# Kernel tuning notes

Measured on AMD Instinct MI355X. Metric: run time of the kernel, lower is better.

The kernel has to match this reference:

```python
import jax, jax.numpy as jnp
import numpy as np


def setup_inputs() -> dict:
    key = jax.random.key(0)
    T, B, I, H = 512, 64, 512, 512
    k = 1.0 / np.sqrt(H)
    ks = jax.random.split(key, 5)
    x = jax.random.normal(ks[0], (T, B, I), dtype=jnp.float32)
    w_ih = jax.random.uniform(ks[1], (H, I), jnp.float32, -k, k)
    w_hh = jax.random.uniform(ks[2], (H, H), jnp.float32, -k, k)
    b_ih = jax.random.uniform(ks[3], (H,), jnp.float32, -k, k)
    b_hh = jax.random.uniform(ks[4], (H,), jnp.float32, -k, k)
    return {"x": x, "w_ih": w_ih, "w_hh": w_hh, "b_ih": b_ih, "b_hh": b_hh}


def reference(x, w_ih, w_hh, b_ih, b_hh):
    # Single-layer Elman RNN, batch_first=False: x is [T, B, I].
    # h_t = tanh(x_t @ W_ih^T + b_ih + h_{t-1} @ W_hh^T + b_hh)
    T, B, _ = x.shape
    H = w_hh.shape[0]
    # Precompute input projections for all timesteps in one big GEMM.
    xproj = jnp.einsum('tbi,hi->tbh', x, w_ih) + b_ih + b_hh  # [T, B, H]

    def step(h, xp_t):
        h_new = jnp.tanh(xp_t + h @ w_hh.T)
        return h_new, h_new

    h0 = jnp.zeros((B, H), dtype=x.dtype)
    h_n, output = jax.lax.scan(step, h0, xproj)
    # torch-style h_n has a leading num_layers dim
    return output, h_n[None]
```

## Files before the change

kernel.cpp:

```cpp
#include <hip/hip_runtime.h>
#include <hip/hip_fp16.h>

#define T_STEPS 512
#define BATCH   64
#define HID     512

#define SCH_REG  40
#define SCH_LDS  10
#define SCH_SA   7
#define SCH_SB   7

#define X16_OFF   0u
#define X16_BYTES (16777216u * 2u)
#define WIH_OFF   (X16_OFF + X16_BYTES)
#define WIH_BYTES (262144u * 2u)
#define WHH_OFF   (WIH_OFF + WIH_BYTES)
#define WHH_BYTES (262144u * 2u)
#define WS_FULL   (WHH_OFF + WHH_BYTES)

typedef _Float16 half2v  __attribute__((ext_vector_type(2)));
typedef short    short8  __attribute__((ext_vector_type(8)));
typedef float    f32x4   __attribute__((ext_vector_type(4)));
union F4H { float4 f; half2v h[4]; };

__device__ inline float dot2f(half2v a, half2v b, float c) {
    return __builtin_amdgcn_fdot2(a, b, c, false);
}
__device__ inline unsigned short f2bf(float f) {
    unsigned u = __builtin_bit_cast(unsigned, f);
    return (unsigned short)((u + 0x7FFFu + ((u >> 16) & 1u)) >> 16);
}

__global__ __launch_bounds__(256) void cvt_f16(const float* __restrict__ w,
                                               __half* __restrict__ o) {
    const int i = (blockIdx.x * 256 + threadIdx.x) * 4;
    float4 v = *(const float4*)(w + i);
    __half2 p0; p0.x = __float2half(v.x); p0.y = __float2half(v.y);
    __half2 p1; p1.x = __float2half(v.z); p1.y = __float2half(v.w);
    *(__half2*)(o + i)     = p0;
    *(__half2*)(o + i + 2) = p1;
}

__global__ __launch_bounds__(256) void cvt_bf16(const float* __restrict__ s,
                                                unsigned short* __restrict__ o) {
    const int i = (blockIdx.x * 256 + threadIdx.x) * 4;
    float4 v = *(const float4*)(s + i);
    ushort4 r = {f2bf(v.x), f2bf(v.y), f2bf(v.z), f2bf(v.w)};
    *(ushort4*)(o + i) = r;
}

__global__ __launch_bounds__(256) void xproj_mfma(
    const unsigned short* __restrict__ x16,
    const unsigned short* __restrict__ w16,
    const float* __restrict__ b_ih, const float* __restrict__ b_hh,
    float* __restrict__ out)
{
    __shared__ __align__(16) unsigned short As[128][40];
    __shared__ __align__(16) unsigned short Bs[128][40];

    const int tid   = threadIdx.x;
    const int mBase = blockIdx.y * 128;
    const int nBase = blockIdx.x * 128;
    const int wave  = tid >> 6, lane = tid & 63;
    const int wy    = wave >> 1, wx = wave & 1;
    const int quad  = lane >> 4, l15 = lane & 15;
    const int lr    = tid >> 2;
    const int lk    = (tid & 3) * 8;

    f32x4 acc[4][4] = {};

    const size_t arow0 = (size_t)(mBase + lr) * 512 + lk;
    const size_t brow0 = (size_t)(nBase + lr) * 512 + lk;

    for (int k0 = 0; k0 < 512; k0 += 32) {
        int4 a0 = *(const int4*)(x16 + arow0 + k0);
        int4 a1 = *(const int4*)(x16 + arow0 + (size_t)64 * 512 + k0);
        int4 b0 = *(const int4*)(w16 + brow0 + k0);
        int4 b1 = *(const int4*)(w16 + brow0 + (size_t)64 * 512 + k0);
        __syncthreads();
        *(int4*)&As[lr][lk]      = a0;
        *(int4*)&As[lr + 64][lk] = a1;
        *(int4*)&Bs[lr][lk]      = b0;
        *(int4*)&Bs[lr + 64][lk] = b1;
        __syncthreads();

        short8 af[4], bf[4];
#pragma unroll
        for (int mt = 0; mt < 4; ++mt)
            af[mt] = *(const short8*)&As[wy * 64 + mt * 16 + l15][quad * 8];
#pragma unroll
        for (int nt = 0; nt < 4; ++nt)
            bf[nt] = *(const short8*)&Bs[wx * 64 + nt * 16 + l15][quad * 8];
#pragma unroll
        for (int mt = 0; mt < 4; ++mt)
#pragma unroll
            for (int nt = 0; nt < 4; ++nt)
                acc[mt][nt] = __builtin_amdgcn_mfma_f32_16x16x32_bf16(
                    af[mt], bf[nt], acc[mt][nt], 0, 0, 0);
    }

    float bias[4]; int coln[4];
#pragma unroll
    for (int nt = 0; nt < 4; ++nt) {
        coln[nt] = nBase + wx * 64 + nt * 16 + l15;
        bias[nt] = b_ih[coln[nt]] + b_hh[coln[nt]];
    }
#pragma unroll
    for (int mt = 0; mt < 4; ++mt)
#pragma unroll
        for (int r = 0; r < 4; ++r) {
            const int row = mBase + wy * 64 + mt * 16 + quad * 4 + r;
#pragma unroll
            for (int nt = 0; nt < 4; ++nt)
                out[(size_t)row * 512 + coln[nt]] = acc[mt][nt][r] + bias[nt];
        }
}

__global__ __launch_bounds__(256) void xproj_gemm(
    const float* __restrict__ x, const float* __restrict__ w_ih,
    const float* __restrict__ b_ih, const float* __restrict__ b_hh,
    float* __restrict__ out)
{
    __shared__ __align__(16) float As[16][68];
    __shared__ __align__(16) float Bs[16][68];

    const int tid   = threadIdx.x;
    const int tx    = tid & 15;
    const int ty    = tid >> 4;
    const int mBase = blockIdx.y * 64;
    const int nBase = blockIdx.x * 64;
    const int ldr   = tid >> 2;
    const int ldk   = (tid & 3) * 4;

    float acc[4][4] = {};
    const float* aptr = x    + (size_t)(mBase + ldr) * 512 + ldk;
    const float* bptr = w_ih + (size_t)(nBase + ldr) * 512 + ldk;

    for (int k0 = 0; k0 < 512; k0 += 16) {
        float4 av = *(const float4*)(aptr + k0);
        float4 bv = *(const float4*)(bptr + k0);
        __syncthreads();
        As[ldk + 0][ldr] = av.x; As[ldk + 1][ldr] = av.y;
        As[ldk + 2][ldr] = av.z; As[ldk + 3][ldr] = av.w;
        Bs[ldk + 0][ldr] = bv.x; Bs[ldk + 1][ldr] = bv.y;
        Bs[ldk + 2][ldr] = bv.z; Bs[ldk + 3][ldr] = bv.w;
        __syncthreads();
#pragma unroll
        for (int kk = 0; kk < 16; ++kk) {
            float4 a = *(const float4*)&As[kk][ty * 4];
            float4 b = *(const float4*)&Bs[kk][tx * 4];
            float ar[4] = {a.x, a.y, a.z, a.w};
            float br[4] = {b.x, b.y, b.z, b.w};
#pragma unroll
            for (int i = 0; i < 4; ++i)
#pragma unroll
                for (int j = 0; j < 4; ++j)
                    acc[i][j] = fmaf(ar[i], br[j], acc[i][j]);
        }
    }
    const int n0 = nBase + tx * 4;
    float bias[4];
#pragma unroll
    for (int j = 0; j < 4; ++j) bias[j] = b_ih[n0 + j] + b_hh[n0 + j];
#pragma unroll
    for (int i = 0; i < 4; ++i) {
        const int m = mBase + ty * 4 + i;
        float4 v = {acc[i][0] + bias[0], acc[i][1] + bias[1],
                    acc[i][2] + bias[2], acc[i][3] + bias[3]};
        *(float4*)(out + (size_t)m * 512 + n0) = v;
    }
}

#define ACC4(WF, G) do {                                        \
    F4H hh_; hh_.f = *(const float4*)(hrow + (G) * 8);          \
    F4H ww_; ww_.f = (WF);                                      \
    a0 = dot2f(ww_.h[0], hh_.h[0], a0);                         \
    a1 = dot2f(ww_.h[1], hh_.h[1], a1);                         \
    a2 = dot2f(ww_.h[2], hh_.h[2], a2);                         \
    a3 = dot2f(ww_.h[3], hh_.h[3], a3); } while (0)

__global__ __launch_bounds__(512)
__attribute__((amdgpu_waves_per_eu(2, 2)))
void rnn_scan4(const __half* __restrict__ w16, float* __restrict__ out)
{
    __shared__ __align__(16) float4 wlds[SCH_LDS][HID];
    __shared__ __align__(16) __half hbuf[2][HID];

    const int b = blockIdx.x;
    const int j = threadIdx.x;

    const __half* wrow = w16 + (size_t)j * HID;

    float4 wreg[SCH_REG];
#pragma unroll
    for (int c = 0; c < SCH_REG; ++c)
        wreg[c] = *(const float4*)(wrow + c * 8);

#pragma unroll
    for (int c = 0; c < SCH_LDS; ++c)
        wlds[c][j] = *(const float4*)(wrow + (SCH_REG + c) * 8);

    hbuf[0][j] = __float2half(0.f);
    __syncthreads();

    float* outb = out + (size_t)b * HID + j;
    const size_t stride = (size_t)BATCH * HID;
    const __half* wstr = wrow + (SCH_REG + SCH_LDS) * 8;

    int cur = 0;
    float hn = 0.f;
    float xp_next = outb[0];

    for (int t = 0; t < T_STEPS; ++t) {
        const float xp = xp_next;
        const int tn = (t + 1 < T_STEPS) ? (t + 1) : t;
        xp_next = outb[(size_t)tn * stride];

        const __half* hrow = hbuf[cur];

        float4 wa[SCH_SA];
#pragma unroll
        for (int c = 0; c < SCH_SA; ++c)
            wa[c] = *(const float4*)(wstr + c * 8);

        float a0 = xp, a1 = 0.f, a2 = 0.f, a3 = 0.f;

#pragma unroll
        for (int c = 0; c < 20; ++c) ACC4(wreg[c], c);

#pragma unroll
        for (int c = 0; c < SCH_SA; ++c)
            ACC4(wa[c], SCH_REG + SCH_LDS + c);

        float4 wb[SCH_SB];
#pragma unroll
        for (int c = 0; c < SCH_SB; ++c)
            wb[c] = *(const float4*)(wstr + (SCH_SA + c) * 8);

#pragma unroll
        for (int c = 20; c < SCH_REG; ++c) ACC4(wreg[c], c);
#pragma unroll
        for (int c = 0; c < SCH_LDS; ++c) {
            float4 wf = wlds[c][j];
            ACC4(wf, SCH_REG + c);
        }

#pragma unroll
        for (int c = 0; c < SCH_SB; ++c)
            ACC4(wb[c], SCH_REG + SCH_LDS + SCH_SA + c);

        float s = (a0 + a1) + (a2 + a3);
        s = fminf(fmaxf(s, -15.f), 15.f);
        const float e = __expf(2.f * s);
        hn = (e - 1.f) * __builtin_amdgcn_rcpf(e + 1.f);

        outb[(size_t)t * stride] = hn;
        hbuf[cur ^ 1][j] = __float2half(hn);
        __syncthreads();
        cur ^= 1;
    }
    out[(size_t)T_STEPS * stride + (size_t)b * HID + j] = hn;
}

__global__ __launch_bounds__(512) void rnn_scan_f32(const float* __restrict__ w,
                                                    float* __restrict__ out)
{
    __shared__ __align__(16) __half hs[2][HID];
    const int b = blockIdx.x;
    const int j = threadIdx.x;

    hs[0][j] = __float2half(0.f);
    __syncthreads();

    const float* wrow32 = w + (size_t)j * HID;
    float* outb = out + (size_t)b * HID + j;
    int cur = 0;
    float hn = 0.f;

    for (int t = 0; t < T_STEPS; ++t) {
        float a0 = outb[(size_t)t * (BATCH * HID)];
        float a1 = 0.f, a2 = 0.f, a3 = 0.f;
#pragma unroll 4
        for (int k0 = 0; k0 < HID; k0 += 8) {
            float4 w0 = *(const float4*)(wrow32 + k0);
            float4 w1 = *(const float4*)(wrow32 + k0 + 4);
            F4H h; h.f = *(const float4*)(&hs[cur][k0]);
            float2 h0 = __half22float2(*(__half2*)&h.h[0]);
            float2 h1 = __half22float2(*(__half2*)&h.h[1]);
            float2 h2 = __half22float2(*(__half2*)&h.h[2]);
            float2 h3 = __half22float2(*(__half2*)&h.h[3]);
            a0 = fmaf(w0.x, h0.x, a0); a1 = fmaf(w0.y, h0.y, a1);
            a2 = fmaf(w0.z, h1.x, a2); a3 = fmaf(w0.w, h1.y, a3);
            a0 = fmaf(w1.x, h2.x, a0); a1 = fmaf(w1.y, h2.y, a1);
            a2 = fmaf(w1.z, h3.x, a2); a3 = fmaf(w1.w, h3.y, a3);
        }
        hn = tanhf((a0 + a1) + (a2 + a3));
        outb[(size_t)t * (BATCH * HID)] = hn;
        hs[cur ^ 1][j] = __float2half(hn);
        __syncthreads();
        cur ^= 1;
    }
    out[(size_t)T_STEPS * BATCH * HID + (size_t)b * HID + j] = hn;
}

extern "C" void kernel_launch(void* const* d_in, const int* in_sizes, int n_in,
                              void* d_out, int out_size, void* d_ws, size_t ws_size,
                              hipStream_t stream) {
    const float* x    = (const float*)d_in[0];
    const float* w_ih = (const float*)d_in[1];
    const float* w_hh = (const float*)d_in[2];
    const float* b_ih = (const float*)d_in[3];
    const float* b_hh = (const float*)d_in[4];
    float* out = (float*)d_out;

    char* ws = (char*)d_ws;
    const bool full = ws_size >= (size_t)WS_FULL;
    const bool mid  = ws_size >= (size_t)WHH_BYTES;

    if (full) {
        unsigned short* x16   = (unsigned short*)(ws + X16_OFF);
        unsigned short* wih16 = (unsigned short*)(ws + WIH_OFF);
        __half*         whh16 = (__half*)(ws + WHH_OFF);
        cvt_bf16<<<16384, 256, 0, stream>>>(x, x16);
        cvt_bf16<<<256,   256, 0, stream>>>(w_ih, wih16);
        cvt_f16 <<<256,   256, 0, stream>>>(w_hh, whh16);
        xproj_mfma<<<dim3(4, 256), 256, 0, stream>>>(x16, wih16, b_ih, b_hh, out);
        rnn_scan4<<<BATCH, HID, 0, stream>>>(whh16, out);
    } else if (mid) {
        __half* whh16 = (__half*)ws;
        cvt_f16<<<256, 256, 0, stream>>>(w_hh, whh16);
        xproj_gemm<<<dim3(8, 512), 256, 0, stream>>>(x, w_ih, b_ih, b_hh, out);
        rnn_scan4<<<BATCH, HID, 0, stream>>>(whh16, out);
    } else {
        xproj_gemm<<<dim3(8, 512), 256, 0, stream>>>(x, w_ih, b_ih, b_hh, out);
        rnn_scan_f32<<<BATCH, HID, 0, stream>>>(w_hh, out);
    }
}
```

Before: 892.5 us.

## Fuse x bf16 conversion into GEMM and transpose W_hh for coalesced streaming

The separate pass that converts x to bf16 is removed, and the GEMM now loads fp32 x and converts it while staging into LDS. This drops a 32MB write and a 32MB read of the temporary. W_hh is converted into a chunk-major transposed fp16 layout so that per-step weight streaming in the scan is coalesced across threads. The register/LDS split in the scan is rebalanced (36 register chunks, 14 LDS chunks), with asm barriers to keep the weights pinned in VGPRs. The workspace path and the middle fallback are simplified.

```diff
diff --git a/kernel.cpp b/kernel.cpp
--- a/kernel.cpp
+++ b/kernel.cpp
@@ -5,18 +5,16 @@
 #define BATCH   64
 #define HID     512
 
-#define SCH_REG  40
-#define SCH_LDS  10
-#define SCH_SA   7
-#define SCH_SB   7
-
-#define X16_OFF   0u
-#define X16_BYTES (16777216u * 2u)
-#define WIH_OFF   (X16_OFF + X16_BYTES)
+#define SR  36
+#define SL  14
+#define SSA 7
+#define SSB 7
+
+#define WIH_OFF   0u
 #define WIH_BYTES (262144u * 2u)
-#define WHH_OFF   (WIH_OFF + WIH_BYTES)
-#define WHH_BYTES (262144u * 2u)
-#define WS_FULL   (WHH_OFF + WHH_BYTES)
+#define WHHT_OFF  (WIH_OFF + WIH_BYTES)
+#define WHHT_BYTES (262144u * 2u)
+#define WS_FULL   (WHHT_OFF + WHHT_BYTES)
 
 typedef _Float16 half2v  __attribute__((ext_vector_type(2)));
 typedef short    short8  __attribute__((ext_vector_type(8)));
@@ -29,16 +27,6 @@
 __device__ inline unsigned short f2bf(float f) {
     unsigned u = __builtin_bit_cast(unsigned, f);
     return (unsigned short)((u + 0x7FFFu + ((u >> 16) & 1u)) >> 16);
-}
-
-__global__ __launch_bounds__(256) void cvt_f16(const float* __restrict__ w,
-                                               __half* __restrict__ o) {
-    const int i = (blockIdx.x * 256 + threadIdx.x) * 4;
-    float4 v = *(const float4*)(w + i);
-    __half2 p0; p0.x = __float2half(v.x); p0.y = __float2half(v.y);
-    __half2 p1; p1.x = __float2half(v.z); p1.y = __float2half(v.w);
-    *(__half2*)(o + i)     = p0;
-    *(__half2*)(o + i + 2) = p1;
 }
 
 __global__ __launch_bounds__(256) void cvt_bf16(const float* __restrict__ s,
@@ -49,8 +37,23 @@
     *(ushort4*)(o + i) = r;
 }
 
-__global__ __launch_bounds__(256) void xproj_mfma(
-    const unsigned short* __restrict__ x16,
+__global__ __launch_bounds__(256) void cvt_whhT(const float* __restrict__ w,
+                                                __half* __restrict__ o) {
+    const int idx = blockIdx.x * 256 + threadIdx.x;
+    const int c = idx >> 9;
+    const int r = idx & 511;
+    float4 v0 = *(const float4*)(w + (size_t)r * 512 + c * 8);
+    float4 v1 = *(const float4*)(w + (size_t)r * 512 + c * 8 + 4);
+    __half2 p0; p0.x = __float2half(v0.x); p0.y = __float2half(v0.y);
+    __half2 p1; p1.x = __float2half(v0.z); p1.y = __float2half(v0.w);
+    __half2 p2; p2.x = __float2half(v1.x); p2.y = __float2half(v1.y);
+    __half2 p3; p3.x = __float2half(v1.z); p3.y = __float2half(v1.w);
+    __half2* dst = (__half2*)(o + (size_t)idx * 8);
+    dst[0] = p0; dst[1] = p1; dst[2] = p2; dst[3] = p3;
+}
+
+__global__ __launch_bounds__(256) void xproj_mfma2(
+    const float* __restrict__ x,
     const unsigned short* __restrict__ w16,
     const float* __restrict__ b_ih, const float* __restrict__ b_hh,
     float* __restrict__ out)
@@ -73,13 +76,23 @@
     const size_t brow0 = (size_t)(nBase + lr) * 512 + lk;
 
     for (int k0 = 0; k0 < 512; k0 += 32) {
-        int4 a0 = *(const int4*)(x16 + arow0 + k0);
-        int4 a1 = *(const int4*)(x16 + arow0 + (size_t)64 * 512 + k0);
+        float4 xa0 = *(const float4*)(x + arow0 + k0);
+        float4 xa1 = *(const float4*)(x + arow0 + k0 + 4);
+        float4 xb0 = *(const float4*)(x + arow0 + (size_t)64 * 512 + k0);
+        float4 xb1 = *(const float4*)(x + arow0 + (size_t)64 * 512 + k0 + 4);
         int4 b0 = *(const int4*)(w16 + brow0 + k0);
         int4 b1 = *(const int4*)(w16 + brow0 + (size_t)64 * 512 + k0);
         __syncthreads();
-        *(int4*)&As[lr][lk]      = a0;
-        *(int4*)&As[lr + 64][lk] = a1;
+        {
+            ushort4 p0 = {f2bf(xa0.x), f2bf(xa0.y), f2bf(xa0.z), f2bf(xa0.w)};
+            ushort4 p1 = {f2bf(xa1.x), f2bf(xa1.y), f2bf(xa1.z), f2bf(xa1.w)};
+            ushort4 p2 = {f2bf(xb0.x), f2bf(xb0.y), f2bf(xb0.z), f2bf(xb0.w)};
+            ushort4 p3 = {f2bf(xb1.x), f2bf(xb1.y), f2bf(xb1.z), f2bf(xb1.w)};
+            *(ushort4*)&As[lr][lk]          = p0;
+            *(ushort4*)&As[lr][lk + 4]      = p1;
+            *(ushort4*)&As[lr + 64][lk]     = p2;
+            *(ushort4*)&As[lr + 64][lk + 4] = p3;
+        }
         *(int4*)&Bs[lr][lk]      = b0;
         *(int4*)&Bs[lr + 64][lk] = b1;
         __syncthreads();
@@ -180,74 +193,78 @@
     a3 = dot2f(ww_.h[3], hh_.h[3], a3); } while (0)
 
 __global__ __launch_bounds__(512)
-__attribute__((amdgpu_waves_per_eu(2, 2)))
-void rnn_scan4(const __half* __restrict__ w16, float* __restrict__ out)
+__attribute__((amdgpu_waves_per_eu(2, 2), amdgpu_num_vgpr(256)))
+void rnn_scan5(const __half* __restrict__ wT, float* __restrict__ out)
 {
-    __shared__ __align__(16) float4 wlds[SCH_LDS][HID];
+    __shared__ __align__(16) float4 wlds[SL][HID];
     __shared__ __align__(16) __half hbuf[2][HID];
 
     const int b = blockIdx.x;
     const int j = threadIdx.x;
 
-    const __half* wrow = w16 + (size_t)j * HID;
-
-    float4 wreg[SCH_REG];
-#pragma unroll
-    for (int c = 0; c < SCH_REG; ++c)
-        wreg[c] = *(const float4*)(wrow + c * 8);
-
-#pragma unroll
-    for (int c = 0; c < SCH_LDS; ++c)
-        wlds[c][j] = *(const float4*)(wrow + (SCH_REG + c) * 8);
+    float4 wreg[SR];
+#pragma unroll
+    for (int c = 0; c < SR; ++c)
+        wreg[c] = *(const float4*)(wT + ((size_t)c * HID + j) * 8);
+
+#pragma unroll
+    for (int c = 0; c < SL; ++c)
+        wlds[c][j] = *(const float4*)(wT + ((size_t)(SR + c) * HID + j) * 8);
 
     hbuf[0][j] = __float2half(0.f);
     __syncthreads();
 
     float* outb = out + (size_t)b * HID + j;
     const size_t stride = (size_t)BATCH * HID;
-    const __half* wstr = wrow + (SCH_REG + SCH_LDS) * 8;
+    const __half* wstr = wT + ((size_t)(SR + SL) * HID + j) * 8;
+    const size_t cstride = (size_t)HID * 8;
 
     int cur = 0;
     float hn = 0.f;
     float xp_next = outb[0];
 
     for (int t = 0; t < T_STEPS; ++t) {
+#pragma unroll
+        for (int c = 0; c < SR; ++c)
+            asm volatile("" : "+v"(wreg[c].x), "+v"(wreg[c].y),
+                              "+v"(wreg[c].z), "+v"(wreg[c].w));
+
         const float xp = xp_next;
         const int tn = (t + 1 < T_STEPS) ? (t + 1) : t;
         xp_next = outb[(size_t)tn * stride];
 
         const __half* hrow = hbuf[cur];
 
-        float4 wa[SCH_SA];
-#pragma unroll
-        for (int c = 0; c < SCH_SA; ++c)
-            wa[c] = *(const float4*)(wstr + c * 8);
+        float4 wa[SSA];
+#pragma unroll
+        for (int c = 0; c < SSA; ++c)
+            wa[c] = *(const float4*)(wstr + (size_t)c * cstride);
 
         float a0 = xp, a1 = 0.f, a2 = 0.f, a3 = 0.f;
 
 #pragma unroll
-        for (int c = 0; c < 20; ++c) ACC4(wreg[c], c);
-
-#pragma unroll
-        for (int c = 0; c < SCH_SA; ++c)
-            ACC4(wa[c], SCH_REG + SCH_LDS + c);
-
-        float4 wb[SCH_SB];
-#pragma unroll
-        for (int c = 0; c < SCH_SB; ++c)
-            wb[c] = *(const float4*)(wstr + (SCH_SA + c) * 8);
-
-#pragma unroll
-        for (int c = 20; c < SCH_REG; ++c) ACC4(wreg[c], c);
-#pragma unroll
-        for (int c = 0; c < SCH_LDS; ++c) {
+        for (int c = 0; c < 18; ++c) ACC4(wreg[c], c);
+
+#pragma unroll
+        for (int c = 0; c < SSA; ++c)
+            ACC4(wa[c], SR + SL + c);
+
+        float4 wb[SSB];
+#pragma unroll
+        for (int c = 0; c < SSB; ++c)
+            wb[c] = *(const float4*)(wstr + (size_t)(SSA + c) * cstride);
+
+#pragma unroll
+        for (int c = 18; c < SR; ++c) ACC4(wreg[c], c);
+#pragma unroll
+        for (int c = 0; c < SL; ++c) {
             float4 wf = wlds[c][j];
-            ACC4(wf, SCH_REG + c);
-        }
-
-#pragma unroll
-        for (int c = 0; c < SCH_SB; ++c)
-            ACC4(wb[c], SCH_REG + SCH_LDS + SCH_SA + c);
+            ACC4(wf, SR + c);
+        }
+
+#pragma unroll
+        for (int c = 0; c < SSB; ++c)
+            ACC4(wb[c], SR + SL + SSA + c);
 
         float s = (a0 + a1) + (a2 + a3);
         s = fminf(fmaxf(s, -15.f), 15.f);
@@ -314,23 +331,13 @@
     float* out = (float*)d_out;
 
     char* ws = (char*)d_ws;
-    const bool full = ws_size >= (size_t)WS_FULL;
-    const bool mid  = ws_size >= (size_t)WHH_BYTES;
-
-    if (full) {
-        unsigned short* x16   = (unsigned short*)(ws + X16_OFF);
+    if (ws_size >= (size_t)WS_FULL) {
         unsigned short* wih16 = (unsigned short*)(ws + WIH_OFF);
-        __half*         whh16 = (__half*)(ws + WHH_OFF);
-        cvt_bf16<<<16384, 256, 0, stream>>>(x, x16);
-        cvt_bf16<<<256,   256, 0, stream>>>(w_ih, wih16);
-        cvt_f16 <<<256,   256, 0, stream>>>(w_hh, whh16);
-        xproj_mfma<<<dim3(4, 256), 256, 0, stream>>>(x16, wih16, b_ih, b_hh, out);
-        rnn_scan4<<<BATCH, HID, 0, stream>>>(whh16, out);
-    } else if (mid) {
-        __half* whh16 = (__half*)ws;
-        cvt_f16<<<256, 256, 0, stream>>>(w_hh, whh16);
-        xproj_gemm<<<dim3(8, 512), 256, 0, stream>>>(x, w_ih, b_ih, b_hh, out);
-        rnn_scan4<<<BATCH, HID, 0, stream>>>(whh16, out);
+        __half*         whhT  = (__half*)(ws + WHHT_OFF);
+        cvt_bf16<<<256, 256, 0, stream>>>(w_ih, wih16);
+        cvt_whhT<<<128, 256, 0, stream>>>(w_hh, whhT);
+        xproj_mfma2<<<dim3(4, 256), 256, 0, stream>>>(x, wih16, b_ih, b_hh, out);
+        rnn_scan5<<<BATCH, HID, 0, stream>>>(whhT, out);
     } else {
         xproj_gemm<<<dim3(8, 512), 256, 0, stream>>>(x, w_ih, b_ih, b_hh, out);
         rnn_scan_f32<<<BATCH, HID, 0, stream>>>(w_hh, out);
```

Measured after the change: 1.449 ms. +62.4%, slower.
